# Performance work log

Hardware: AMD Instinct MI355X
Metric: run time of the kernel (lower is better)

## Reference

```python
import jax, jax.numpy as jnp
import numpy as np

B, C, H, W = 32, 256, 32, 32
C8 = C // 8


def setup_inputs() -> dict:
    key = jax.random.key(0)
    ks = jax.random.split(key, 8)
    s = 1.0 / np.sqrt(C)
    return {
        "x": jax.random.normal(ks[0], (B, C, H, W), dtype=jnp.float32),
        "Wq": jax.random.normal(ks[1], (C8, C), dtype=jnp.float32) * s,
        "bq": jax.random.normal(ks[2], (C8,), dtype=jnp.float32) * s,
        "Wk": jax.random.normal(ks[3], (C8, C), dtype=jnp.float32) * s,
        "bk": jax.random.normal(ks[4], (C8,), dtype=jnp.float32) * s,
        "Wv": jax.random.normal(ks[5], (C, C), dtype=jnp.float32) * s,
        "bv": jax.random.normal(ks[6], (C,), dtype=jnp.float32) * s,
        "gamma": jax.random.normal(ks[7], (1,), dtype=jnp.float32) * 0.1,
    }


def reference(x, Wq, bq, Wk, bk, Wv, bv, gamma):
    b, c, h, w = x.shape
    n = h * w
    xf = x.reshape(b, c, n)  # [B, C, N]
    # 1x1 convs == per-pixel linear projections
    q = jnp.einsum('dc,bcn->bnd', Wq, xf) + bq            # [B, N, C/8]
    k = jnp.einsum('dc,bcn->bdn', Wk, xf) + bk[:, None]    # [B, C/8, N]
    v = jnp.einsum('dc,bcn->bdn', Wv, xf) + bv[:, None]    # [B, C, N]
    energy = jnp.einsum('bnd,bdm->bnm', q, k)              # [B, N, N], no scaling (as in source)
    attn = jax.nn.softmax(energy, axis=-1)                 # softmax over keys
    # out[:, :, i] = sum_j V[:, :, j] * attn[i, j]
    out = jnp.einsum('bdn,bmn->bdm', v, attn)              # [B, C, N]
    out = out.reshape(b, c, h, w)
    return gamma * out + x
```

## Files before the change

kernel.cpp:

```cpp
#include <hip/hip_runtime.h>
#include <math.h>

#define BB 32
#define CC 256
#define CQ 32
#define NN 1024

typedef short bf16x8 __attribute__((ext_vector_type(8)));
typedef float f32x4  __attribute__((ext_vector_type(4)));
typedef unsigned short u16;

__device__ __forceinline__ u16 f2bf(float f) {
    unsigned u = __float_as_uint(f);
    u = (u + 0x7FFFu + ((u >> 16) & 1u)) >> 16;
    return (u16)u;
}

__global__ void wpack_kernel(const float* __restrict__ Wq,
                             const float* __restrict__ Wk,
                             const float* __restrict__ Wv,
                             u16* __restrict__ wfrag)
{
    const int o = blockIdx.x * 256 + threadIdx.x;
    const int j    = o & 7;
    const int lane = (o >> 3) & 63;
    const int kc   = (o >> 9) & 7;
    const int rt   = o >> 12;
    const int row  = rt * 16 + (lane & 15);
    const int col  = kc * 32 + (lane >> 4) * 8 + j;
    const float v = (row < 32) ? Wq[row * 256 + col]
                  : (row < 64) ? Wk[(row - 32) * 256 + col]
                               : Wv[(row - 64) * 256 + col];
    wfrag[o] = f2bf(v);
}

struct QSmem {
    union {
        u16 xs[64][272];
        u16 osv[CC][72];
    };
    u16 osqk[64][72];
};

__global__ __launch_bounds__(256, 2) void qkv_kernel(
    const float* __restrict__ x, const u16* __restrict__ wfrag,
    const float* __restrict__ bq, const float* __restrict__ bk,
    const float* __restrict__ bv,
    u16* __restrict__ qt, u16* __restrict__ kt, u16* __restrict__ vv)
{
    __shared__ QSmem sm;
    const int b = blockIdx.y, n0 = blockIdx.x * 64;
    const int t = threadIdx.x;
    const int lane = t & 63, w = t >> 6;
    const int quad = lane >> 4, c16 = lane & 15;

    {
        const float* xb = x + (size_t)b * CC * NN + n0;
        const int cg = t >> 4;
        const int n4 = (t & 15) * 4;
        float4 f[16];
#pragma unroll
        for (int it = 0; it < 16; ++it)
            f[it] = *(const float4*)(xb + (size_t)(it * 16 + cg) * NN + n4);
#pragma unroll
        for (int it = 0; it < 16; ++it) {
            const int c = it * 16 + cg;
            sm.xs[n4 + 0][c] = f2bf(f[it].x);
            sm.xs[n4 + 1][c] = f2bf(f[it].y);
            sm.xs[n4 + 2][c] = f2bf(f[it].z);
            sm.xs[n4 + 3][c] = f2bf(f[it].w);
        }
    }
    __syncthreads();

    f32x4 acc[5][4];
#pragma unroll
    for (int i = 0; i < 5; ++i)
#pragma unroll
        for (int j = 0; j < 4; ++j) acc[i][j] = (f32x4){0.f, 0.f, 0.f, 0.f};

#pragma unroll 2
    for (int k = 0; k < 8; ++k) {
        const int c0 = k * 32;
        bf16x8 wa[5], xb[4];
#pragma unroll
        for (int rs = 0; rs < 5; ++rs)
            wa[rs] = *(const bf16x8*)&wfrag[(size_t)(((w * 5 + rs) * 8 + k) * 64 + lane) * 8];
#pragma unroll
        for (int ns = 0; ns < 4; ++ns)
            xb[ns] = *(const bf16x8*)&sm.xs[ns * 16 + c16][c0 + quad * 8];
#pragma unroll
        for (int rs = 0; rs < 5; ++rs)
#pragma unroll
            for (int ns = 0; ns < 4; ++ns)
                acc[rs][ns] = __builtin_amdgcn_mfma_f32_16x16x32_bf16(
                    wa[rs], xb[ns], acc[rs][ns], 0, 0, 0);
    }

    __syncthreads();

#pragma unroll
    for (int rs = 0; rs < 5; ++rs) {
#pragma unroll
        for (int r = 0; r < 4; ++r) {
            const int rg = w * 80 + rs * 16 + quad * 4 + r;
            const float bias = (rg < 32) ? bq[rg] : (rg < 64) ? bk[rg - 32] : bv[rg - 64];
#pragma unroll
            for (int ns = 0; ns < 4; ++ns) {
                const int n = ns * 16 + c16;
                const u16 h = f2bf(acc[rs][ns][r] + bias);
                if (rg < 64) sm.osqk[n][rg] = h;
                else         sm.osv[rg - 64][n] = h;
            }
        }
    }
    __syncthreads();

    {
        u16* dst = (w >= 2) ? kt : qt;
        const int dof = (w >= 2) ? 32 : 0;
        const int wl = w & 1;
        const size_t base = ((size_t)b * NN + n0) * CQ;
#pragma unroll
        for (int it = 0; it < 4; ++it) {
            const int o = wl * 2048 + it * 512 + lane * 8;
            const int n = o >> 5, d = o & 31;
            const bf16x8 v = *(const bf16x8*)&sm.osqk[n][d + dof];
            *(bf16x8*)&dst[base + o] = v;
        }
    }
#pragma unroll
    for (int it = 0; it < 8; ++it) {
        const int o = it * 2048 + t * 8;
        const int c = o >> 6, n = o & 63;
        const bf16x8 v = *(const bf16x8*)&sm.osv[c][n];
        *(bf16x8*)&vv[((size_t)b * CC + c) * NN + n0 + n] = v;
    }
}

__global__ __launch_bounds__(256, 2) void attn_kernel(
    const u16* __restrict__ qt, const u16* __restrict__ kt,
    const u16* __restrict__ vv, const float* __restrict__ x,
    const float* __restrict__ gamma_p, float* __restrict__ out)
{
    __shared__ float ps[2][64][68];

    const int bid  = blockIdx.x;
    const int xcd  = bid & 7;
    const int slot = bid >> 3;
    const int b    = (xcd << 2) | (slot >> 4);
    const int m0   = (slot & 15) * 64;

    const int t = threadIdx.x, lane = t & 63, w = t >> 6;
    const int quad = lane >> 4, c16 = lane & 15;

    const bf16x8 qa = *(const bf16x8*)&qt[((size_t)b * NN + m0 + w * 16 + c16) * CQ + quad * 8];

    bf16x8 ones;
#pragma unroll
    for (int j = 0; j < 8; ++j) ones[j] = (short)0x3F80;

    f32x4 accO[4][4];
    f32x4 lsum[4];
#pragma unroll
    for (int i = 0; i < 4; ++i) {
        lsum[i] = (f32x4){0.f, 0.f, 0.f, 0.f};
#pragma unroll
        for (int j = 0; j < 4; ++j) accO[i][j] = (f32x4){0.f, 0.f, 0.f, 0.f};
    }

    const u16* vbase = vv + (size_t)b * CC * NN;
    const u16* kbase = kt + (size_t)b * NN * CQ;

    bf16x8 kb[4];
#pragma unroll
    for (int s = 0; s < 4; ++s)
        kb[s] = *(const bf16x8*)&kbase[(size_t)(s * 16 + c16) * CQ + quad * 8];

    for (int step = 0; step < 16; ++step) {
        const int nbase = step * 64;
        float* psb = &ps[step & 1][0][0];

        bf16x8 va[4][2];
#pragma unroll
        for (int cs = 0; cs < 4; ++cs)
#pragma unroll
            for (int kc = 0; kc < 2; ++kc)
                va[cs][kc] = *(const bf16x8*)&vbase[
                    (size_t)(w * 64 + cs * 16 + c16) * NN + nbase + kc * 32 + quad * 8];

        f32x4 accS[4];
#pragma unroll
        for (int s = 0; s < 4; ++s)
            accS[s] = __builtin_amdgcn_mfma_f32_16x16x32_bf16(
                qa, kb[s], (f32x4){0.f, 0.f, 0.f, 0.f}, 0, 0, 0);

#pragma unroll
        for (int r = 0; r < 4; ++r)
#pragma unroll
            for (int s = 0; s < 4; ++s)
                psb[(w * 16 + quad * 4 + r) * 68 + s * 16 + c16] = __expf(accS[s][r]);

        if (step < 15) {
#pragma unroll
            for (int s = 0; s < 4; ++s)
                kb[s] = *(const bf16x8*)&kbase[(size_t)(nbase + 64 + s * 16 + c16) * CQ + quad * 8];
        }

        __syncthreads();

#pragma unroll
        for (int ms = 0; ms < 4; ++ms) {
            bf16x8 pb[2];
#pragma unroll
            for (int kc = 0; kc < 2; ++kc) {
                const f32x4 p0 = *(const f32x4*)&psb[(ms * 16 + c16) * 68 + kc * 32 + quad * 8];
                const f32x4 p1 = *(const f32x4*)&psb[(ms * 16 + c16) * 68 + kc * 32 + quad * 8 + 4];
                bf16x8 pk;
                pk[0] = (short)f2bf(p0[0]); pk[1] = (short)f2bf(p0[1]);
                pk[2] = (short)f2bf(p0[2]); pk[3] = (short)f2bf(p0[3]);
                pk[4] = (short)f2bf(p1[0]); pk[5] = (short)f2bf(p1[1]);
                pk[6] = (short)f2bf(p1[2]); pk[7] = (short)f2bf(p1[3]);
                pb[kc] = pk;
            }
            lsum[ms] = __builtin_amdgcn_mfma_f32_16x16x32_bf16(ones, pb[0], lsum[ms], 0, 0, 0);
            lsum[ms] = __builtin_amdgcn_mfma_f32_16x16x32_bf16(ones, pb[1], lsum[ms], 0, 0, 0);
#pragma unroll
            for (int cs = 0; cs < 4; ++cs) {
#pragma unroll
                for (int kc = 0; kc < 2; ++kc)
                    accO[cs][ms] = __builtin_amdgcn_mfma_f32_16x16x32_bf16(
                        va[cs][kc], pb[kc], accO[cs][ms], 0, 0, 0);
            }
        }
    }

    const float gamma = gamma_p[0];
#pragma unroll
    for (int ms = 0; ms < 4; ++ms) {
        const float inv = gamma / lsum[ms][0];
        const int m = m0 + ms * 16 + c16;
#pragma unroll
        for (int cs = 0; cs < 4; ++cs) {
            const int cbase = w * 64 + cs * 16 + quad * 4;
#pragma unroll
            for (int r = 0; r < 4; ++r) {
                const size_t idx = ((size_t)b * CC + cbase + r) * NN + m;
                out[idx] = accO[cs][ms][r] * inv + x[idx];
            }
        }
    }
}

extern "C" void kernel_launch(void* const* d_in, const int* in_sizes, int n_in,
                              void* d_out, int out_size, void* d_ws, size_t ws_size,
                              hipStream_t stream)
{
    const float* x  = (const float*)d_in[0];
    const float* Wq = (const float*)d_in[1];
    const float* bq = (const float*)d_in[2];
    const float* Wk = (const float*)d_in[3];
    const float* bk = (const float*)d_in[4];
    const float* Wv = (const float*)d_in[5];
    const float* bv = (const float*)d_in[6];
    const float* gm = (const float*)d_in[7];
    float* out = (float*)d_out;

    u16* qt    = (u16*)d_ws;
    u16* kt    = qt + (size_t)BB * NN * CQ;
    u16* vv    = kt + (size_t)BB * NN * CQ;
    u16* wfrag = vv + (size_t)BB * CC * NN;

    wpack_kernel<<<320, 256, 0, stream>>>(Wq, Wk, Wv, wfrag);
    dim3 grid(16, BB);
    qkv_kernel<<<grid, 256, 0, stream>>>(x, wfrag, bq, bk, bv, qt, kt, vv);
    attn_kernel<<<512, 256, 0, stream>>>(qt, kt, vv, x, gm, out);
}
```

Measured before the change: 157.2 us.

## Prefetch V tiles one step ahead and store bf16 probabilities in swizzled LDS

```diff
diff --git a/kernel.cpp b/kernel.cpp
--- a/kernel.cpp
+++ b/kernel.cpp
@@ -36,7 +36,7 @@
 
 struct QSmem {
     union {
-        u16 xs[64][272];
+        u16 xs[64][268];
         u16 osv[CC][72];
     };
     u16 osqk[64][72];
@@ -56,19 +56,17 @@
 
     {
         const float* xb = x + (size_t)b * CC * NN + n0;
-        const int cg = t >> 4;
-        const int n4 = (t & 15) * 4;
-        float4 f[16];
-#pragma unroll
-        for (int it = 0; it < 16; ++it)
-            f[it] = *(const float4*)(xb + (size_t)(it * 16 + cg) * NN + n4);
-#pragma unroll
-        for (int it = 0; it < 16; ++it) {
-            const int c = it * 16 + cg;
-            sm.xs[n4 + 0][c] = f2bf(f[it].x);
-            sm.xs[n4 + 1][c] = f2bf(f[it].y);
-            sm.xs[n4 + 2][c] = f2bf(f[it].z);
-            sm.xs[n4 + 3][c] = f2bf(f[it].w);
+        const int n2 = 2 * (lane & 31);
+        const int cr = w * 2 + (lane >> 5);
+        float2 f[32];
+#pragma unroll
+        for (int it = 0; it < 32; ++it)
+            f[it] = *(const float2*)(xb + (size_t)(it * 8 + cr) * NN + n2);
+#pragma unroll
+        for (int it = 0; it < 32; ++it) {
+            const int c = it * 8 + cr;
+            sm.xs[n2 + 0][c] = f2bf(f[it].x);
+            sm.xs[n2 + 1][c] = f2bf(f[it].y);
         }
     }
     __syncthreads();
@@ -87,8 +85,14 @@
         for (int rs = 0; rs < 5; ++rs)
             wa[rs] = *(const bf16x8*)&wfrag[(size_t)(((w * 5 + rs) * 8 + k) * 64 + lane) * 8];
 #pragma unroll
-        for (int ns = 0; ns < 4; ++ns)
-            xb[ns] = *(const bf16x8*)&sm.xs[ns * 16 + c16][c0 + quad * 8];
+        for (int ns = 0; ns < 4; ++ns) {
+            const short4 a = *(const short4*)&sm.xs[ns * 16 + c16][c0 + quad * 8];
+            const short4 b2 = *(const short4*)&sm.xs[ns * 16 + c16][c0 + quad * 8 + 4];
+            bf16x8 v;
+            v[0] = a.x; v[1] = a.y; v[2] = a.z; v[3] = a.w;
+            v[4] = b2.x; v[5] = b2.y; v[6] = b2.z; v[7] = b2.w;
+            xb[ns] = v;
+        }
 #pragma unroll
         for (int rs = 0; rs < 5; ++rs)
 #pragma unroll
@@ -143,7 +147,7 @@
     const u16* __restrict__ vv, const float* __restrict__ x,
     const float* __restrict__ gamma_p, float* __restrict__ out)
 {
-    __shared__ float ps[2][64][68];
+    __shared__ u16 ps16[2][64][72];
 
     const int bid  = blockIdx.x;
     const int xcd  = bid & 7;
@@ -153,6 +157,9 @@
 
     const int t = threadIdx.x, lane = t & 63, w = t >> 6;
     const int quad = lane >> 4, c16 = lane & 15;
+    const int ch   = c16 >> 3;
+    const int c7   = c16 & 7;
+    const int qkey = (c16 >> 2) & 3;
 
     const bf16x8 qa = *(const bf16x8*)&qt[((size_t)b * NN + m0 + w * 16 + c16) * CQ + quad * 8];
 
@@ -177,17 +184,17 @@
     for (int s = 0; s < 4; ++s)
         kb[s] = *(const bf16x8*)&kbase[(size_t)(s * 16 + c16) * CQ + quad * 8];
 
-    for (int step = 0; step < 16; ++step) {
+    bf16x8 vaA[4][2], vaB[4][2];
+#pragma unroll
+    for (int cs = 0; cs < 4; ++cs)
+#pragma unroll
+        for (int kc = 0; kc < 2; ++kc)
+            vaA[cs][kc] = *(const bf16x8*)&vbase[
+                (size_t)(w * 64 + cs * 16 + c16) * NN + kc * 32 + quad * 8];
+
+    auto STEP = [&](int step, bf16x8 (&vc)[4][2], bf16x8 (&vn)[4][2]) {
         const int nbase = step * 64;
-        float* psb = &ps[step & 1][0][0];
-
-        bf16x8 va[4][2];
-#pragma unroll
-        for (int cs = 0; cs < 4; ++cs)
-#pragma unroll
-            for (int kc = 0; kc < 2; ++kc)
-                va[cs][kc] = *(const bf16x8*)&vbase[
-                    (size_t)(w * 64 + cs * 16 + c16) * NN + nbase + kc * 32 + quad * 8];
+        u16* psb = &ps16[step & 1][0][0];
 
         f32x4 accS[4];
 #pragma unroll
@@ -195,11 +202,14 @@
             accS[s] = __builtin_amdgcn_mfma_f32_16x16x32_bf16(
                 qa, kb[s], (f32x4){0.f, 0.f, 0.f, 0.f}, 0, 0, 0);
 
+        const int rowb = w * 16 + quad * 4;
 #pragma unroll
         for (int r = 0; r < 4; ++r)
 #pragma unroll
-            for (int s = 0; s < 4; ++s)
-                psb[(w * 16 + quad * 4 + r) * 68 + s * 16 + c16] = __expf(accS[s][r]);
+            for (int s = 0; s < 4; ++s) {
+                const int nb = (2 * s + ch) ^ quad;
+                psb[(rowb + r) * 72 + nb * 8 + c7] = f2bf(__expf(accS[s][r]));
+            }
 
         if (step < 15) {
 #pragma unroll
@@ -209,20 +219,22 @@
 
         __syncthreads();
 
+        if (step < 15) {
+#pragma unroll
+            for (int cs = 0; cs < 4; ++cs)
+#pragma unroll
+                for (int kc = 0; kc < 2; ++kc)
+                    vn[cs][kc] = *(const bf16x8*)&vbase[
+                        (size_t)(w * 64 + cs * 16 + c16) * NN + nbase + 64 + kc * 32 + quad * 8];
+        }
+
 #pragma unroll
         for (int ms = 0; ms < 4; ++ms) {
             bf16x8 pb[2];
 #pragma unroll
-            for (int kc = 0; kc < 2; ++kc) {
-                const f32x4 p0 = *(const f32x4*)&psb[(ms * 16 + c16) * 68 + kc * 32 + quad * 8];
-                const f32x4 p1 = *(const f32x4*)&psb[(ms * 16 + c16) * 68 + kc * 32 + quad * 8 + 4];
-                bf16x8 pk;
-                pk[0] = (short)f2bf(p0[0]); pk[1] = (short)f2bf(p0[1]);
-                pk[2] = (short)f2bf(p0[2]); pk[3] = (short)f2bf(p0[3]);
-                pk[4] = (short)f2bf(p1[0]); pk[5] = (short)f2bf(p1[1]);
-                pk[6] = (short)f2bf(p1[2]); pk[7] = (short)f2bf(p1[3]);
-                pb[kc] = pk;
-            }
+            for (int kc = 0; kc < 2; ++kc)
+                pb[kc] = *(const bf16x8*)&psb[(ms * 16 + c16) * 72
+                                              + (4 * kc + (quad ^ qkey)) * 8];
             lsum[ms] = __builtin_amdgcn_mfma_f32_16x16x32_bf16(ones, pb[0], lsum[ms], 0, 0, 0);
             lsum[ms] = __builtin_amdgcn_mfma_f32_16x16x32_bf16(ones, pb[1], lsum[ms], 0, 0, 0);
 #pragma unroll
@@ -230,9 +242,14 @@
 #pragma unroll
                 for (int kc = 0; kc < 2; ++kc)
                     accO[cs][ms] = __builtin_amdgcn_mfma_f32_16x16x32_bf16(
-                        va[cs][kc], pb[kc], accO[cs][ms], 0, 0, 0);
-            }
-        }
+                        vc[cs][kc], pb[kc], accO[cs][ms], 0, 0, 0);
+            }
+        }
+    };
+
+    for (int it = 0; it < 8; ++it) {
+        STEP(2 * it,     vaA, vaB);
+        STEP(2 * it + 1, vaB, vaA);
     }
 
     const float gamma = gamma_p[0];
```

New measurement: 155.9 us. No clear change (-0.8%).
